# Kernel tuning notes

Measured on AMD Instinct MI355X. Metric: run time of the kernel, lower is better.

Reference implementation:

```python
import jax, jax.numpy as jnp
import numpy as np

HEADS = 16
DIM_HEAD = 64
DIM = 1024
SEQ = 2048
BATCH = 1
THR_MIN = 0.01
THR_MAX = 0.9
LN_EPS = 1e-5
NEG = -jnp.finfo(jnp.float32).max


def _ln(x, gamma):
    # torch F.layer_norm over last dim, beta fixed to zeros
    mu = jnp.mean(x, axis=-1, keepdims=True)
    var = jnp.mean(jnp.square(x - mu), axis=-1, keepdims=True)
    return (x - mu) * jax.lax.rsqrt(var + LN_EPS) * gamma


def setup_inputs() -> dict:
    key = jax.random.key(0)
    ks = jax.random.split(key, 8)
    s = 0.02  # realistic init scale for weights
    return {
        "x": jax.random.normal(ks[0], (BATCH, SEQ, DIM), jnp.float32),
        "gamma_norm": jnp.ones((DIM,), jnp.float32),
        "Wq": jax.random.normal(ks[1], (DIM, HEADS * DIM_HEAD), jnp.float32) * s,
        "Wk": jax.random.normal(ks[2], (DIM, HEADS * DIM_HEAD), jnp.float32) * s,
        "Wv": jax.random.normal(ks[3], (DIM, HEADS * DIM_HEAD), jnp.float32) * s,
        "Wout": jax.random.normal(ks[4], (HEADS * DIM_HEAD, DIM), jnp.float32) * s,
        "gamma_out": jnp.ones((DIM,), jnp.float32),
        "W_gcn0": jax.random.normal(ks[5], (DIM_HEAD, DIM_HEAD), jnp.float32) * s,
        "b_gcn0": jnp.zeros((DIM_HEAD,), jnp.float32),
        "W_gcn1": jax.random.normal(ks[6], (DIM_HEAD, DIM_HEAD), jnp.float32) * s,
        "b_gcn1": jnp.zeros((DIM_HEAD,), jnp.float32),
        "W_lin": jax.random.normal(ks[7], (DIM_HEAD, DIM_HEAD), jnp.float32) * s,
        "b_lin": jnp.zeros((DIM_HEAD,), jnp.float32),
    }


def reference(x, gamma_norm, Wq, Wk, Wv, Wout, gamma_out,
              W_gcn0, b_gcn0, W_gcn1, b_gcn1, W_lin, b_lin):
    b, n, _ = x.shape
    h, d = HEADS, DIM_HEAD
    scale = d ** -0.5

    xn = _ln(x, gamma_norm)
    # projections, split heads: b n (h d) -> b h n d
    q = (xn @ Wq).reshape(b, n, h, d).transpose(0, 2, 1, 3) * scale
    k = (xn @ Wk).reshape(b, n, h, d).transpose(0, 2, 1, 3)
    v = (xn @ Wv).reshape(b, n, h, d).transpose(0, 2, 1, 3)

    sim = jnp.einsum("bhid,bhjd->bhij", q, k)
    causal_mask = jnp.triu(jnp.ones((n, n), bool), 1)
    sim = jnp.where(causal_mask, NEG, sim)
    attn = jax.nn.softmax(sim.astype(jnp.float32), axis=-1)  # [b,h,n,n]

    out = jnp.einsum("bhij,bhjd->bhid", attn, v)

    # --- attention-derived adjacency GCN path ---
    adj = attn.reshape(b * h, n, n) + jnp.eye(n, dtype=attn.dtype)
    adj = jnp.clip(adj, 0.0, 1.0)
    adj = jnp.where(adj < THR_MIN, 0.0, adj)
    adj = jnp.where(adj > THR_MAX, 1.0, adj)

    g = v.reshape(b * h, n, d)
    deg = jnp.sum(adj, axis=-1, keepdims=True)  # [bh, n, 1]
    # GCN layer 0 (skip connection, exact GELU like nn.GELU())
    g = jax.nn.gelu(jnp.matmul(adj, g @ W_gcn0 + b_gcn0) / deg + g, approximate=False)
    # GCN layer 1
    g = jax.nn.gelu(jnp.matmul(adj, g @ W_gcn1 + b_gcn1) / deg + g, approximate=False)
    # final linear (dropout inactive in eval)
    g = g @ W_lin + b_lin

    out = out + g.reshape(b, h, n, d)

    # merge heads: b h n d -> b n (h d), output projection + LayerNorm
    out = out.transpose(0, 2, 1, 3).reshape(b, n, h * d)
    out = _ln(out @ Wout, gamma_out)
    return out
```

## Files before the change

### kernel.cpp

```cpp
#include <hip/hip_runtime.h>
#include <hip/hip_bf16.h>
#include <math.h>
#include <stdint.h>

#define DEV __device__ __forceinline__

typedef unsigned short u16;
typedef __attribute__((ext_vector_type(8))) short s16x8;
typedef __attribute__((ext_vector_type(4))) float f32x4;
typedef __attribute__((ext_vector_type(16))) float f32x16;
typedef __attribute__((ext_vector_type(4))) unsigned u32x4;

static constexpr int SEQ = 2048;
static constexpr int DIM = 1024;
static constexpr int HEADS = 16;
static constexpr int QKVLD = 3072;
static constexpr int TOT32 = 2080;

DEV u16 f2bf(float f) {
  unsigned u = __float_as_uint(f);
  u = u + 0x7FFFu + ((u >> 16) & 1u);
  return (u16)(u >> 16);
}
DEV float bf2f(u16 b) { return __uint_as_float(((unsigned)b) << 16); }
DEV float gelu_exact(float x) { return 0.5f * x * (1.0f + erff(x * 0.70710678118654752f)); }

DEV unsigned pkbf(float lo, float hi) {
  __hip_bfloat162 h = __float22bfloat162_rn(make_float2(lo, hi));
  unsigned r; __builtin_memcpy(&r, &h, 4); return r;
}

#define MFMA16(a, b, c) __builtin_amdgcn_mfma_f32_16x16x32_bf16(a, b, c, 0, 0, 0)
#define MFMA32(a, b, c) __builtin_amdgcn_mfma_f32_32x32x16_bf16(a, b, c, 0, 0, 0)

DEV s16x8 u4_to_s8(u32x4 u) { union { u32x4 a; s16x8 b; } c; c.a = u; return c.b; }

DEV float tsum16(const float* v) {
  float a0 = v[0] + v[1], a1 = v[2] + v[3], a2 = v[4] + v[5], a3 = v[6] + v[7];
  float a4 = v[8] + v[9], a5 = v[10] + v[11], a6 = v[12] + v[13], a7 = v[14] + v[15];
  float b0 = a0 + a1, b1 = a2 + a3, b2 = a4 + a5, b3 = a6 + a7;
  return (b0 + b1) + (b2 + b3);
}
DEV float tsum8(const float* v) {
  float a0 = v[0] + v[1], a1 = v[2] + v[3], a2 = v[4] + v[5], a3 = v[6] + v[7];
  return (a0 + a1) + (a2 + a3);
}

DEV void build_frags(const float* p, int hi, s16x8* fr) {
  unsigned pw[4][2];
#pragma unroll
  for (int rq = 0; rq < 4; ++rq) {
    pw[rq][0] = pkbf(p[4 * rq + 0], p[4 * rq + 1]);
    pw[rq][1] = pkbf(p[4 * rq + 2], p[4 * rq + 3]);
  }
#pragma unroll
  for (int m = 0; m < 2; ++m) {
    unsigned x0 = __shfl_xor(pw[2 * m + 1][0], 32);
    unsigned x1 = __shfl_xor(pw[2 * m + 1][1], 32);
    unsigned y0 = __shfl_xor(pw[2 * m][0], 32);
    unsigned y1 = __shfl_xor(pw[2 * m][1], 32);
    u32x4 u;
    u[0] = hi ? x0 : pw[2 * m][0];
    u[1] = hi ? x1 : pw[2 * m][1];
    u[2] = hi ? pw[2 * m + 1][0] : y0;
    u[3] = hi ? pw[2 * m + 1][1] : y1;
    fr[m] = u4_to_s8(u);
  }
}

__global__ __launch_bounds__(256) void ln_rows_f32(const float* __restrict__ in,
                                                   const float* __restrict__ gamma,
                                                   float* __restrict__ outp) {
  int row = blockIdx.x;
  const float* x = in + (size_t)row * DIM;
  float v[4];
  float s = 0.f;
#pragma unroll
  for (int e = 0; e < 4; ++e) { v[e] = x[threadIdx.x + 256 * e]; s += v[e]; }
  __shared__ float red[8];
  int lane = threadIdx.x & 63, wid = threadIdx.x >> 6;
#pragma unroll
  for (int off = 32; off; off >>= 1) s += __shfl_xor(s, off);
  if (lane == 0) red[wid] = s;
  __syncthreads();
  float mean = (red[0] + red[1] + red[2] + red[3]) * (1.0f / DIM);
  float vs = 0.f;
#pragma unroll
  for (int e = 0; e < 4; ++e) { float d = v[e] - mean; vs += d * d; }
#pragma unroll
  for (int off = 32; off; off >>= 1) vs += __shfl_xor(vs, off);
  __syncthreads();
  if (lane == 0) red[wid] = vs;
  __syncthreads();
  float var = (red[0] + red[1] + red[2] + red[3]) * (1.0f / DIM);
  float rstd = rsqrtf(var + 1e-5f);
#pragma unroll
  for (int e = 0; e < 4; ++e) {
    int c = threadIdx.x + 256 * e;
    outp[(size_t)row * DIM + c] = (v[e] - mean) * rstd * gamma[c];
  }
}

__global__ __launch_bounds__(256) void prep1(
    const float* __restrict__ x, const float* __restrict__ gamma_n, u16* __restrict__ xn,
    const float* __restrict__ Wq, const float* __restrict__ Wk, const float* __restrict__ Wv,
    const float* __restrict__ Wout, const float* __restrict__ Wg0,
    const float* __restrict__ Wg1, const float* __restrict__ Wlin,
    u16* __restrict__ WqkvT, u16* __restrict__ WoT,
    u16* __restrict__ Wg0T, u16* __restrict__ Wg1T, u16* __restrict__ WlinT) {
  int bid = blockIdx.x;
  __shared__ float tile[64][65];
  __shared__ float red[8];
  if (bid < 2048) {
    int row = bid;
    const float* xr = x + (size_t)row * DIM;
    float v[4];
    float s = 0.f;
#pragma unroll
    for (int e = 0; e < 4; ++e) { v[e] = xr[threadIdx.x + 256 * e]; s += v[e]; }
    int lane = threadIdx.x & 63, wid = threadIdx.x >> 6;
#pragma unroll
    for (int off = 32; off; off >>= 1) s += __shfl_xor(s, off);
    if (lane == 0) red[wid] = s;
    __syncthreads();
    float mean = (red[0] + red[1] + red[2] + red[3]) * (1.0f / DIM);
    float vs = 0.f;
#pragma unroll
    for (int e = 0; e < 4; ++e) { float d = v[e] - mean; vs += d * d; }
#pragma unroll
    for (int off = 32; off; off >>= 1) vs += __shfl_xor(vs, off);
    __syncthreads();
    if (lane == 0) red[wid] = vs;
    __syncthreads();
    float var = (red[0] + red[1] + red[2] + red[3]) * (1.0f / DIM);
    float rstd = rsqrtf(var + 1e-5f);
#pragma unroll
    for (int e = 0; e < 4; ++e) {
      int c = threadIdx.x + 256 * e;
      xn[(size_t)row * DIM + c] = f2bf((v[e] - mean) * rstd * gamma_n[c]);
    }
    return;
  }
  int wb = bid - 2048;
  const float* src; u16* dst; int R, C, c0, r0;
  if (wb < 1024) {
    int z = wb >> 8, rem = wb & 255;
    src = (z == 0) ? Wq : (z == 1) ? Wk : (z == 2) ? Wv : Wout;
    dst = (z == 0) ? WqkvT : (z == 1) ? WqkvT + (size_t)DIM * DIM
        : (z == 2) ? WqkvT + (size_t)2 * DIM * DIM : WoT;
    R = DIM; C = DIM; c0 = (rem & 15) * 64; r0 = (rem >> 4) * 64;
  } else {
    int k = wb - 1024;
    src = (k == 0) ? Wg0 : (k == 1) ? Wg1 : Wlin;
    dst = (k == 0) ? Wg0T : (k == 1) ? Wg1T : WlinT;
    R = 64; C = 64; c0 = 0; r0 = 0;
  }
  int tx = threadIdx.x & 63, ty = threadIdx.x >> 6;
  for (int rr = ty; rr < 64; rr += 4)
    tile[rr][tx] = src[(size_t)(r0 + rr) * C + c0 + tx];
  __syncthreads();
  for (int rr = ty; rr < 64; rr += 4)
    dst[(size_t)(c0 + rr) * R + r0 + tx] = f2bf(tile[tx][rr]);
}

__global__ __launch_bounds__(256) void prep2(
    const u16* __restrict__ QKV, u16* __restrict__ Kp, u16* __restrict__ Vp,
    const u16* __restrict__ Wg0T, const float* __restrict__ bg0, u16* __restrict__ H0p) {
  int bid = blockIdx.x;
  int tid = threadIdx.x, wid = tid >> 6, lane = tid & 63;
  __shared__ u16 t[16][72];
  __shared__ __align__(16) u16 Ws[64][72];
  __shared__ __align__(16) u16 tt[64][72];
  if (bid < 3072) {
    int bx = bid >> 4, h = bid & 15;
    int l31 = lane & 31, hi = lane >> 5;
    if (bx < 64) {
      int jb = bx, fi = wid;
      s16x8 v = *(const s16x8*)(QKV + (size_t)(jb * 32 + l31) * QKVLD + 1024 + h * 64 + fi * 16 + hi * 8);
      *(s16x8*)(Kp + ((size_t)(h * 64 + jb) * 4 + fi) * 512 + lane * 8) = v;
    } else {
      int jb16 = bx - 64;
      if (tid < 128) {
        int r = tid >> 3, c = (tid & 7) * 8;
        *(s16x8*)&t[r][c] = *(const s16x8*)(QKV + (size_t)(jb16 * 16 + r) * QKVLD + 2048 + h * 64 + c);
      }
      __syncthreads();
      if (wid < 2) {
        int dh = wid;
        s16x8 v;
#pragma unroll
        for (int e = 0; e < 8; ++e) v[e] = (short)t[hi * 8 + e][dh * 32 + l31];
        *(s16x8*)(Vp + ((size_t)(h * 128 + jb16) * 2 + dh) * 512 + lane * 8) = v;
      }
    }
    return;
  }
  int tb = bid - 3072;
  int bx = tb >> 4, h = tb & 15;
  int l15 = lane & 15, lhi = lane >> 4;
  {
    int r = tid >> 2, cc = (tid & 3) * 8;
    *(s16x8*)&Ws[r][cc] = *(const s16x8*)(Wg0T + r * 64 + cc);
    *(s16x8*)&Ws[r][cc + 32] = *(const s16x8*)(Wg0T + r * 64 + cc + 32);
  }
  __syncthreads();
  int j = bx * 64 + wid * 16 + l15;
  const u16* arow = QKV + (size_t)j * QKVLD + 2048 + h * 64;
  s16x8 a0 = *(const s16x8*)(arow + lhi * 8);
  s16x8 a1 = *(const s16x8*)(arow + 32 + lhi * 8);
  f32x4 acc[4];
#pragma unroll
  for (int c = 0; c < 4; ++c) {
    acc[c] = f32x4{0.f, 0.f, 0.f, 0.f};
    s16x8 b0 = *(const s16x8*)&Ws[c * 16 + l15][lhi * 8];
    s16x8 b1 = *(const s16x8*)&Ws[c * 16 + l15][32 + lhi * 8];
    acc[c] = MFMA16(a0, b0, acc[c]);
    acc[c] = MFMA16(a1, b1, acc[c]);
  }
  int rl = wid * 16 + lhi * 4;
#pragma unroll
  for (int c = 0; c < 4; ++c)
#pragma unroll
    for (int r = 0; r < 4; ++r)
      tt[rl + r][c * 16 + l15] = f2bf(acc[c][r] + bg0[c * 16 + l15]);
  __syncthreads();
  int l31 = lane & 31, hi = lane >> 5;
#pragma unroll
  for (int dh = 0; dh < 2; ++dh) {
    s16x8 v;
#pragma unroll
    for (int e = 0; e < 8; ++e) v[e] = (short)tt[wid * 16 + hi * 8 + e][dh * 32 + l31];
    *(s16x8*)(H0p + ((size_t)(h * 128 + bx * 4 + wid) * 2 + dh) * 512 + lane * 8) = v;
  }
}

__global__ __launch_bounds__(256) void gemm_pack(
    const u16* __restrict__ Asrc, int ld, const u16* __restrict__ Wt,
    const float* __restrict__ bias, u16* __restrict__ Hp) {
  int bx = blockIdx.x, h = blockIdx.y;
  __shared__ __align__(16) u16 Ws[64][72];
  __shared__ __align__(16) u16 tt[64][72];
  int tid = threadIdx.x, lane = tid & 63, wid = tid >> 6;
  int l15 = lane & 15, lhi = lane >> 4;
  {
    int r = tid >> 2, cc = (tid & 3) * 8;
    *(s16x8*)&Ws[r][cc] = *(const s16x8*)(Wt + r * 64 + cc);
    *(s16x8*)&Ws[r][cc + 32] = *(const s16x8*)(Wt + r * 64 + cc + 32);
  }
  __syncthreads();
  int j = bx * 64 + wid * 16 + l15;
  const u16* arow = Asrc + (size_t)j * ld + h * 64;
  s16x8 a0 = *(const s16x8*)(arow + lhi * 8);
  s16x8 a1 = *(const s16x8*)(arow + 32 + lhi * 8);
  f32x4 acc[4];
#pragma unroll
  for (int c = 0; c < 4; ++c) {
    acc[c] = f32x4{0.f, 0.f, 0.f, 0.f};
    s16x8 b0 = *(const s16x8*)&Ws[c * 16 + l15][lhi * 8];
    s16x8 b1 = *(const s16x8*)&Ws[c * 16 + l15][32 + lhi * 8];
    acc[c] = MFMA16(a0, b0, acc[c]);
    acc[c] = MFMA16(a1, b1, acc[c]);
  }
  int rl = wid * 16 + lhi * 4;
#pragma unroll
  for (int c = 0; c < 4; ++c)
#pragma unroll
    for (int r = 0; r < 4; ++r)
      tt[rl + r][c * 16 + l15] = f2bf(acc[c][r] + bias[c * 16 + l15]);
  __syncthreads();
  int l31 = lane & 31, hi = lane >> 5;
#pragma unroll
  for (int dh = 0; dh < 2; ++dh) {
    s16x8 v;
#pragma unroll
    for (int e = 0; e < 8; ++e) v[e] = (short)tt[wid * 16 + hi * 8 + e][dh * 32 + l31];
    *(s16x8*)(Hp + ((size_t)(h * 128 + bx * 4 + wid) * 2 + dh) * 512 + lane * 8) = v;
  }
}

DEV void gload_lds16(const u16* g, u16* l) {
  __builtin_amdgcn_global_load_lds(
      (const __attribute__((address_space(1))) unsigned int*)g,
      (__attribute__((address_space(3))) unsigned int*)(unsigned int)(uintptr_t)l,
      16, 0, 0);
}
template<int BM, int BN, bool OUT_F32>
__global__ __launch_bounds__(256) void gemm_t(const u16* __restrict__ A,
                                              const u16* __restrict__ Bt,
                                              void* __restrict__ Cout,
                                              int Nn, int K, int Nq, float qs) {
  constexpr int MI = BM / 32;
  constexpr int NI = BN / 32;
  __shared__ __align__(16) u16 As[BM][64];
  __shared__ __align__(16) u16 Bs[BN][64];
  int tid = threadIdx.x, lane = tid & 63, wid = tid >> 6;
  int l15 = lane & 15, lhi = lane >> 4;
  int nwg = gridDim.x * gridDim.y;
  int flat = blockIdx.y * gridDim.x + blockIdx.x;
  int q8 = nwg >> 3, r8 = nwg & 7;
  int xcd = flat & 7, idx = flat >> 3;
  int wg = (xcd < r8) ? xcd * (q8 + 1) + idx : r8 * (q8 + 1) + (xcd - r8) * q8 + idx;
  int bx = wg % gridDim.x, by = wg / gridDim.x;
  int n0 = bx * BN, m0 = by * BM;
  int wr = wid >> 1, wc = wid & 1;
  float scale = (n0 < Nq) ? qs : 1.0f;
  f32x4 acc[MI][NI];
#pragma unroll
  for (int mi = 0; mi < MI; ++mi)
#pragma unroll
    for (int ni = 0; ni < NI; ++ni) acc[mi][ni] = f32x4{0.f, 0.f, 0.f, 0.f};
  int srow = lane >> 3;
  int scol = ((lane & 7) ^ srow) * 8;
  for (int k0 = 0; k0 < K; k0 += 64) {
    __syncthreads();
#pragma unroll
    for (int i = 0; i < BM / 32; ++i) {
      int row0 = (wid * (BM / 32) + i) * 8;
      gload_lds16(A + (size_t)(m0 + row0 + srow) * K + k0 + scol, &As[row0][0]);
    }
#pragma unroll
    for (int i = 0; i < BN / 32; ++i) {
      int row0 = (wid * (BN / 32) + i) * 8;
      gload_lds16(Bt + (size_t)(n0 + row0 + srow) * K + k0 + scol, &Bs[row0][0]);
    }
    __syncthreads();
#pragma unroll
    for (int ks = 0; ks < 2; ++ks) {
      s16x8 af[MI], bf[NI];
#pragma unroll
      for (int mi = 0; mi < MI; ++mi) {
        int row = wr * (BM / 2) + mi * 16 + l15;
        int c8 = (ks * 4 + lhi) ^ (row & 7);
        af[mi] = *(const s16x8*)&As[row][c8 * 8];
      }
#pragma unroll
      for (int ni = 0; ni < NI; ++ni) {
        int row = wc * (BN / 2) + ni * 16 + l15;
        int c8 = (ks * 4 + lhi) ^ (row & 7);
        bf[ni] = *(const s16x8*)&Bs[row][c8 * 8];
      }
#pragma unroll
      for (int mi = 0; mi < MI; ++mi)
#pragma unroll
        for (int ni = 0; ni < NI; ++ni)
          acc[mi][ni] = MFMA16(af[mi], bf[ni], acc[mi][ni]);
    }
  }
  int orow0 = m0 + wr * (BM / 2), ocol0 = n0 + wc * (BN / 2);
#pragma unroll
  for (int mi = 0; mi < MI; ++mi)
#pragma unroll
    for (int ni = 0; ni < NI; ++ni)
#pragma unroll
      for (int r = 0; r < 4; ++r) {
        int row = orow0 + mi * 16 + lhi * 4 + r;
        int col = ocol0 + ni * 16 + l15;
        float vv = acc[mi][ni][r] * scale;
        if (OUT_F32) ((float*)Cout)[(size_t)row * Nn + col] = vv;
        else         ((u16*)Cout)[(size_t)row * Nn + col] = f2bf(vv);
      }
}

__global__ __launch_bounds__(256) void small_gemm_add(
    const u16* __restrict__ A, int ldo, const u16* __restrict__ Wt,
    const float* __restrict__ bias, const u16* __restrict__ addsrc,
    u16* __restrict__ outp) {
  __shared__ __align__(16) u16 Ws[64][72];
  int tid = threadIdx.x, lane = tid & 63, wid = tid >> 6;
  int l15 = lane & 15, lhi = lane >> 4;
  int m0 = blockIdx.x * 64;
  {
    int r = tid >> 2, cc = (tid & 3) * 8;
    *(s16x8*)&Ws[r][cc] = *(const s16x8*)(Wt + r * 64 + cc);
    *(s16x8*)&Ws[r][cc + 32] = *(const s16x8*)(Wt + r * 64 + cc + 32);
  }
  __syncthreads();
  int R = m0 + wid * 16 + l15;
  const u16* arow = A + (size_t)(R >> 4) * ldo + (R & 15) * 64;
  s16x8 a0 = *(const s16x8*)(arow + lhi * 8);
  s16x8 a1 = *(const s16x8*)(arow + 32 + lhi * 8);
  f32x4 acc[4];
#pragma unroll
  for (int c = 0; c < 4; ++c) {
    acc[c] = f32x4{0.f, 0.f, 0.f, 0.f};
    s16x8 b0 = *(const s16x8*)&Ws[c * 16 + l15][lhi * 8];
    s16x8 b1 = *(const s16x8*)&Ws[c * 16 + l15][32 + lhi * 8];
    acc[c] = MFMA16(a0, b0, acc[c]);
    acc[c] = MFMA16(a1, b1, acc[c]);
  }
  int orow = m0 + wid * 16 + lhi * 4;
#pragma unroll
  for (int c = 0; c < 4; ++c)
#pragma unroll
    for (int r = 0; r < 4; ++r) {
      int col = c * 16 + l15;
      size_t idx = (size_t)(orow + r) * 64 + col;
      outp[idx] = f2bf(acc[c][r] + bias[col] + bf2f(addsrc[idx]));
    }
}

static constexpr float NEGB = -3.0e38f;
DEV int crowf(int r, int hi) { return (r & 3) + 8 * (r >> 2) + 4 * hi; }

__global__ __launch_bounds__(512, 4) void attn_ss(
    const u16* __restrict__ QKV, const u16* __restrict__ Kp, const u16* __restrict__ Vp,
    float* __restrict__ lbuf, u16* __restrict__ oatt, u16* __restrict__ pfS) {
  int tid = threadIdx.x, wq = tid >> 6, lane = tid & 63;
  int l31 = lane & 31, hi = lane >> 5;
  int h = blockIdx.x & 15, sidx = blockIdx.x >> 4;
  int s = 63 - sidx;

  __shared__ float cmb[4][2][16][64];
  __shared__ float slf[8][32];
  __shared__ float sinv[32];

  int qbase = s * 32;
  int cums = (s * (s + 1)) >> 1;
  int n = s + 1;
  int c_lo = (n * wq) >> 3, c_hi = (n * (wq + 1)) >> 3;

  s16x8 qf[4];
#pragma unroll
  for (int fi = 0; fi < 4; ++fi)
    qf[fi] = *(const s16x8*)(QKV + (size_t)(qbase + l31) * QKVLD + h * 64 + fi * 16 + hi * 8);

  f32x16 pv0, pv1;
#pragma unroll
  for (int r = 0; r < 16; ++r) { pv0[r] = 0.f; pv1[r] = 0.f; }
  float lp = 0.f;
  for (int jb = c_lo; jb < c_hi; ++jb) {
    f32x16 sa;
#pragma unroll
    for (int r = 0; r < 16; ++r) sa[r] = 0.f;
#pragma unroll
    for (int fi = 0; fi < 4; ++fi) {
      s16x8 kf = *(const s16x8*)(Kp + ((size_t)(h * 64 + jb) * 4 + fi) * 512 + lane * 8);
      sa = MFMA32(kf, qf[fi], sa);
    }
    bool diag = (jb == s);
    float p[16];
#pragma unroll
    for (int r = 0; r < 16; ++r) {
      float v = sa[r];
      if (diag && (crowf(r, hi) > l31)) v = NEGB;
      p[r] = __expf(v);
    }
    lp += tsum16(p);
    s16x8 pf[2]; build_frags(p, hi, pf);
    size_t fb = ((size_t)h * TOT32 + cums + jb) * 2;
    *(s16x8*)(pfS + fb * 512 + lane * 8) = pf[0];
    *(s16x8*)(pfS + (fb + 1) * 512 + lane * 8) = pf[1];
#pragma unroll
    for (int m = 0; m < 2; ++m) {
      const u16* vb = Vp + ((size_t)(h * 128 + jb * 2 + m) * 2) * 512;
      pv0 = MFMA32(pf[m], *(const s16x8*)(vb + lane * 8), pv0);
      pv1 = MFMA32(pf[m], *(const s16x8*)(vb + 512 + lane * 8), pv1);
    }
  }
  lp += __shfl_xor(lp, 32);
  if (hi == 0) slf[wq][l31] = lp;
  __syncthreads();
  float lt = (slf[0][l31] + slf[1][l31]) + (slf[2][l31] + slf[3][l31]) +
             (slf[4][l31] + slf[5][l31]) + (slf[6][l31] + slf[7][l31]);
  if (wq == 0 && hi == 0) {
    lbuf[(size_t)h * SEQ + qbase + l31] = lt;
    sinv[l31] = 1.0f / lt;
  }
  if (wq >= 4) {
#pragma unroll
    for (int r = 0; r < 16; ++r) {
      cmb[wq - 4][0][r][lane] = pv0[r];
      cmb[wq - 4][1][r][lane] = pv1[r];
    }
  }
  __syncthreads();
  if (wq < 4) {
#pragma unroll
    for (int r = 0; r < 16; ++r) {
      pv0[r] += cmb[wq][0][r][lane];
      pv1[r] += cmb[wq][1][r][lane];
    }
  }
  __syncthreads();
  if (wq == 2 || wq == 3) {
#pragma unroll
    for (int r = 0; r < 16; ++r) {
      cmb[wq - 2][0][r][lane] = pv0[r];
      cmb[wq - 2][1][r][lane] = pv1[r];
    }
  }
  __syncthreads();
  if (wq < 2) {
#pragma unroll
    for (int r = 0; r < 16; ++r) {
      pv0[r] += cmb[wq][0][r][lane];
      pv1[r] += cmb[wq][1][r][lane];
    }
  }
  __syncthreads();
  if (wq == 1) {
#pragma unroll
    for (int r = 0; r < 16; ++r) {
      cmb[0][0][r][lane] = pv0[r];
      cmb[0][1][r][lane] = pv1[r];
    }
  }
  __syncthreads();
  if (wq == 0) {
#pragma unroll
    for (int r = 0; r < 16; ++r) {
      pv0[r] += cmb[0][0][r][lane];
      pv1[r] += cmb[0][1][r][lane];
    }
#pragma unroll
    for (int r = 0; r < 16; ++r) {
      int cr = crowf(r, hi);
      float invl = sinv[cr];
      int qr = qbase + cr;
      oatt[(size_t)qr * DIM + h * 64 + l31] = f2bf(pv0[r] * invl);
      oatt[(size_t)qr * DIM + h * 64 + 32 + l31] = f2bf(pv1[r] * invl);
    }
  }
}

__global__ __launch_bounds__(512, 4) void adjgcn1(
    const u16* __restrict__ QKV, const u16* __restrict__ H0p, u16* __restrict__ adjS,
    const float* __restrict__ lbuf, float* __restrict__ degb,
    unsigned char* __restrict__ maskb, u16* __restrict__ g1) {
  int tid = threadIdx.x, wq = tid >> 6, lane = tid & 63;
  int l31 = lane & 31, hi = lane >> 5;
  int h = blockIdx.x & 15, sidx = blockIdx.x >> 4;
  int s = 63 - sidx;

  __shared__ float cmb[4][2][16][64];
  __shared__ float sdg[8][32];
  __shared__ float sdegf[32];

  int qbase = s * 32;
  int cums = (s * (s + 1)) >> 1;
  int n = s + 1;
  int c_lo = (n * wq) >> 3, c_hi = (n * (wq + 1)) >> 3;

  float invl = 1.0f / lbuf[(size_t)h * SEQ + qbase + l31];

  f32x16 gc0, gc1;
#pragma unroll
  for (int r = 0; r < 16; ++r) { gc0[r] = 0.f; gc1[r] = 0.f; }
  float dacc = 0.f;
  for (int jb = c_lo; jb < c_hi; ++jb) {
    size_t fb = ((size_t)h * TOT32 + cums + jb) * 2;
    s16x8 f0 = *(const s16x8*)(adjS + fb * 512 + lane * 8);
    s16x8 f1 = *(const s16x8*)(adjS + (fb + 1) * 512 + lane * 8);
    bool diag = (jb == s);
    float t0[8], t1[8];
#pragma unroll
    for (int e = 0; e < 8; ++e) {
      float p0 = bf2f((u16)f0[e]) * invl;
      float p1 = bf2f((u16)f1[e]) * invl;
      t0[e] = (p0 < 0.01f) ? 0.f : ((p0 > 0.9f) ? 1.f : p0);
      t1[e] = (p1 < 0.01f) ? 0.f : ((p1 > 0.9f) ? 1.f : p1);
    }
    if (diag) {
#pragma unroll
      for (int e = 0; e < 8; ++e) {
        if (hi * 8 + e == l31) t0[e] = 1.f;
        if (16 + hi * 8 + e == l31) t1[e] = 1.f;
      }
    }
    float as0 = tsum8(t0), as1 = tsum8(t1);
    dacc += as0 + as1;
    unsigned flags = (__ballot(as0 > 0.f) ? 1u : 0u) | (__ballot(as1 > 0.f) ? 2u : 0u);
    s16x8 a0, a1;
#pragma unroll
    for (int e = 0; e < 8; ++e) { a0[e] = (short)f2bf(t0[e]); a1[e] = (short)f2bf(t1[e]); }
    if (flags & 1u) {
      *(s16x8*)(adjS + fb * 512 + lane * 8) = a0;
      const u16* hb = H0p + ((size_t)(h * 128 + jb * 2) * 2) * 512;
      gc0 = MFMA32(a0, *(const s16x8*)(hb + lane * 8), gc0);
      gc1 = MFMA32(a0, *(const s16x8*)(hb + 512 + lane * 8), gc1);
    }
    if (flags & 2u) {
      *(s16x8*)(adjS + (fb + 1) * 512 + lane * 8) = a1;
      const u16* hb = H0p + ((size_t)(h * 128 + jb * 2 + 1) * 2) * 512;
      gc0 = MFMA32(a1, *(const s16x8*)(hb + lane * 8), gc0);
      gc1 = MFMA32(a1, *(const s16x8*)(hb + 512 + lane * 8), gc1);
    }
    if (lane == 0) maskb[(size_t)h * TOT32 + cums + jb] = (unsigned char)flags;
  }
  dacc += __shfl_xor(dacc, 32);
  if (hi == 0) sdg[wq][l31] = dacc;
  if (wq >= 4) {
#pragma unroll
    for (int r = 0; r < 16; ++r) {
      cmb[wq - 4][0][r][lane] = gc0[r];
      cmb[wq - 4][1][r][lane] = gc1[r];
    }
  }
  __syncthreads();
  if (wq < 4) {
#pragma unroll
    for (int r = 0; r < 16; ++r) {
      gc0[r] += cmb[wq][0][r][lane];
      gc1[r] += cmb[wq][1][r][lane];
    }
  }
  __syncthreads();
  if (wq == 2 || wq == 3) {
#pragma unroll
    for (int r = 0; r < 16; ++r) {
      cmb[wq - 2][0][r][lane] = gc0[r];
      cmb[wq - 2][1][r][lane] = gc1[r];
    }
  }
  __syncthreads();
  if (wq < 2) {
#pragma unroll
    for (int r = 0; r < 16; ++r) {
      gc0[r] += cmb[wq][0][r][lane];
      gc1[r] += cmb[wq][1][r][lane];
    }
  }
  __syncthreads();
  if (wq == 1) {
#pragma unroll
    for (int r = 0; r < 16; ++r) {
      cmb[0][0][r][lane] = gc0[r];
      cmb[0][1][r][lane] = gc1[r];
    }
  }
  __syncthreads();
  if (wq == 0) {
    if (hi == 0) {
      float dt = 0.f;
#pragma unroll
      for (int w2 = 0; w2 < 8; ++w2) dt += sdg[w2][l31];
      sdegf[l31] = dt;
      degb[(size_t)h * SEQ + qbase + l31] = dt;
    }
  }
  __syncthreads();
  if (wq == 0) {
#pragma unroll
    for (int r = 0; r < 16; ++r) {
      gc0[r] += cmb[0][0][r][lane];
      gc1[r] += cmb[0][1][r][lane];
    }
#pragma unroll
    for (int r = 0; r < 16; ++r) {
      int cr = crowf(r, hi);
      int qr = qbase + cr;
      float dinv = 1.0f / sdegf[cr];
      float sk0 = bf2f(QKV[(size_t)qr * QKVLD + 2048 + h * 64 + l31]);
      float sk1 = bf2f(QKV[(size_t)qr * QKVLD + 2048 + h * 64 + 32 + l31]);
      g1[(size_t)qr * DIM + h * 64 + l31] = f2bf(gelu_exact(gc0[r] * dinv + sk0));
      g1[(size_t)qr * DIM + h * 64 + 32 + l31] = f2bf(gelu_exact(gc1[r] * dinv + sk1));
    }
  }
}

template<bool READ_ADJ>
__global__ __launch_bounds__(512, 4) void gcn_apply(
    const u16* __restrict__ QKV, const u16* __restrict__ Kp,
    const u16* __restrict__ Hp, const u16* __restrict__ adjS,
    const unsigned char* __restrict__ maskb,
    const float* __restrict__ lbuf, const float* __restrict__ degb,
    const u16* __restrict__ skip, int skipld, u16* __restrict__ outp) {
  int tid = threadIdx.x, wq = tid >> 6, lane = tid & 63;
  int l31 = lane & 31, hi = lane >> 5;
  int h = blockIdx.x & 15, sidx = blockIdx.x >> 4;
  int s = 63 - sidx;

  __shared__ float cmb[4][2][16][64];

  int qbase = s * 32;
  int cums = (s * (s + 1)) >> 1;
  int n = s + 1;
  int c_lo = (n * wq) >> 3, c_hi = (n * (wq + 1)) >> 3;

  f32x16 gc0, gc1;
#pragma unroll
  for (int r = 0; r < 16; ++r) { gc0[r] = 0.f; gc1[r] = 0.f; }

  if constexpr (READ_ADJ) {
    for (int jb = c_lo; jb < c_hi; ++jb) {
      unsigned flags = maskb[(size_t)h * TOT32 + cums + jb];
      if (!flags) continue;
      size_t fb = ((size_t)h * TOT32 + cums + jb) * 2;
#pragma unroll
      for (int m = 0; m < 2; ++m) if ((flags >> m) & 1u) {
        s16x8 af = *(const s16x8*)(adjS + (fb + m) * 512 + lane * 8);
        const u16* hb = Hp + ((size_t)(h * 128 + jb * 2 + m) * 2) * 512;
        gc0 = MFMA32(af, *(const s16x8*)(hb + lane * 8), gc0);
        gc1 = MFMA32(af, *(const s16x8*)(hb + 512 + lane * 8), gc1);
      }
    }
  } else {
    s16x8 qf[4];
#pragma unroll
    for (int fi = 0; fi < 4; ++fi)
      qf[fi] = *(const s16x8*)(QKV + (size_t)(qbase + l31) * QKVLD + h * 64 + fi * 16 + hi * 8);
    float invl = 1.0f / lbuf[(size_t)h * SEQ + qbase + l31];
    for (int jb = c_lo; jb < c_hi; ++jb) {
      unsigned flags = maskb[(size_t)h * TOT32 + cums + jb];
      if (!flags) continue;
      f32x16 sa;
#pragma unroll
      for (int r = 0; r < 16; ++r) sa[r] = 0.f;
#pragma unroll
      for (int fi = 0; fi < 4; ++fi) {
        s16x8 kf = *(const s16x8*)(Kp + ((size_t)(h * 64 + jb) * 4 + fi) * 512 + lane * 8);
        sa = MFMA32(kf, qf[fi], sa);
      }
      bool diag = (jb == s);
      float p[16];
#pragma unroll
      for (int r = 0; r < 16; ++r) {
        int cr = crowf(r, hi);
        float v = sa[r];
        if (diag && (cr > l31)) v = NEGB;
        float pp = __expf(v) * invl;
        p[r] = (diag && (cr == l31)) ? 1.f
               : ((pp < 0.01f) ? 0.f : ((pp > 0.9f) ? 1.f : pp));
      }
      s16x8 af[2]; build_frags(p, hi, af);
#pragma unroll
      for (int m = 0; m < 2; ++m) if ((flags >> m) & 1u) {
        const u16* hb = Hp + ((size_t)(h * 128 + jb * 2 + m) * 2) * 512;
        gc0 = MFMA32(af[m], *(const s16x8*)(hb + lane * 8), gc0);
        gc1 = MFMA32(af[m], *(const s16x8*)(hb + 512 + lane * 8), gc1);
      }
    }
  }

  if (wq >= 4) {
#pragma unroll
    for (int r = 0; r < 16; ++r) {
      cmb[wq - 4][0][r][lane] = gc0[r];
      cmb[wq - 4][1][r][lane] = gc1[r];
    }
  }
  __syncthreads();
  if (wq < 4) {
#pragma unroll
    for (int r = 0; r < 16; ++r) {
      gc0[r] += cmb[wq][0][r][lane];
      gc1[r] += cmb[wq][1][r][lane];
    }
  }
  __syncthreads();
  if (wq == 2 || wq == 3) {
#pragma unroll
    for (int r = 0; r < 16; ++r) {
      cmb[wq - 2][0][r][lane] = gc0[r];
      cmb[wq - 2][1][r][lane] = gc1[r];
    }
  }
  __syncthreads();
  if (wq < 2) {
#pragma unroll
    for (int r = 0; r < 16; ++r) {
      gc0[r] += cmb[wq][0][r][lane];
      gc1[r] += cmb[wq][1][r][lane];
    }
  }
  __syncthreads();
  if (wq == 1) {
#pragma unroll
    for (int r = 0; r < 16; ++r) {
      cmb[0][0][r][lane] = gc0[r];
      cmb[0][1][r][lane] = gc1[r];
    }
  }
  __syncthreads();
  if (wq == 0) {
#pragma unroll
    for (int r = 0; r < 16; ++r) {
      gc0[r] += cmb[0][0][r][lane];
      gc1[r] += cmb[0][1][r][lane];
    }
#pragma unroll
    for (int r = 0; r < 16; ++r) {
      int qr = qbase + crowf(r, hi);
      float dinv = 1.0f / degb[(size_t)h * SEQ + qr];
      float sk0 = bf2f(skip[(size_t)qr * skipld + h * 64 + l31]);
      float sk1 = bf2f(skip[(size_t)qr * skipld + h * 64 + 32 + l31]);
      outp[(size_t)qr * DIM + h * 64 + l31] = f2bf(gelu_exact(gc0[r] * dinv + sk0));
      outp[(size_t)qr * DIM + h * 64 + 32 + l31] = f2bf(gelu_exact(gc1[r] * dinv + sk1));
    }
  }
}

__global__ __launch_bounds__(512, 4) void attn_pv_fb(
    const u16* __restrict__ QKV, const u16* __restrict__ Kp, const u16* __restrict__ Vp,
    float* __restrict__ lbuf, float* __restrict__ degb,
    u16* __restrict__ oatt, unsigned char* __restrict__ maskb) {
  int tid = threadIdx.x, wq = tid >> 6, lane = tid & 63;
  int l31 = lane & 31, hi = lane >> 5;
  int h = blockIdx.x & 15, sidx = blockIdx.x >> 4;
  int s = 63 - sidx;

  __shared__ float cmb[4][2][16][64];
  __shared__ float slf[8][32], sdg[8][32];

  int qbase = s * 32;
  int cums = (s * (s + 1)) >> 1;
  int n = s + 1;
  int c_lo = (n * wq) >> 3, c_hi = (n * (wq + 1)) >> 3;

  s16x8 qf[4];
#pragma unroll
  for (int fi = 0; fi < 4; ++fi)
    qf[fi] = *(const s16x8*)(QKV + (size_t)(qbase + l31) * QKVLD + h * 64 + fi * 16 + hi * 8);

  float lp = 0.f;
  for (int jb = c_lo; jb < c_hi; ++jb) {
    f32x16 sa;
#pragma unroll
    for (int r = 0; r < 16; ++r) sa[r] = 0.f;
#pragma unroll
    for (int fi = 0; fi < 4; ++fi) {
      s16x8 kf = *(const s16x8*)(Kp + ((size_t)(h * 64 + jb) * 4 + fi) * 512 + lane * 8);
      sa = MFMA32(kf, qf[fi], sa);
    }
    bool diag = (jb == s);
    float ev[16];
#pragma unroll
    for (int r = 0; r < 16; ++r) {
      float v = sa[r];
      if (diag && (crowf(r, hi) > l31)) v = NEGB;
      ev[r] = __expf(v);
    }
    lp += tsum16(ev);
  }
  lp += __shfl_xor(lp, 32);
  if (hi == 0) slf[wq][l31] = lp;
  __syncthreads();
  float lt = (slf[0][l31] + slf[1][l31]) + (slf[2][l31] + slf[3][l31]) +
             (slf[4][l31] + slf[5][l31]) + (slf[6][l31] + slf[7][l31]);
  float invl = 1.0f / lt;
  if (wq == 0 && hi == 0) lbuf[(size_t)h * SEQ + qbase + l31] = lt;

  f32x16 pv0, pv1;
#pragma unroll
  for (int r = 0; r < 16; ++r) { pv0[r] = 0.f; pv1[r] = 0.f; }
  float dacc = 0.f;
  for (int jb = c_lo; jb < c_hi; ++jb) {
    f32x16 sa;
#pragma unroll
    for (int r = 0; r < 16; ++r) sa[r] = 0.f;
#pragma unroll
    for (int fi = 0; fi < 4; ++fi) {
      s16x8 kf = *(const s16x8*)(Kp + ((size_t)(h * 64 + jb) * 4 + fi) * 512 + lane * 8);
      sa = MFMA32(kf, qf[fi], sa);
    }
    bool diag = (jb == s);
    float p[16];
#pragma unroll
    for (int r = 0; r < 16; ++r) {
      float v = sa[r];
      if (diag && (crowf(r, hi) > l31)) v = NEGB;
      p[r] = __expf(v) * invl;
    }
    s16x8 pf[2]; build_frags(p, hi, pf);
#pragma unroll
    for (int m = 0; m < 2; ++m) {
      const u16* vb = Vp + ((size_t)(h * 128 + jb * 2 + m) * 2) * 512;
      pv0 = MFMA32(pf[m], *(const s16x8*)(vb + lane * 8), pv0);
      pv1 = MFMA32(pf[m], *(const s16x8*)(vb + 512 + lane * 8), pv1);
    }
#pragma unroll
    for (int r = 0; r < 16; ++r) {
      float pp = p[r];
      p[r] = (diag && (crowf(r, hi) == l31)) ? 1.f
             : ((pp < 0.01f) ? 0.f : ((pp > 0.9f) ? 1.f : pp));
    }
    float as0 = tsum8(&p[0]);
    float as1 = tsum8(&p[8]);
    dacc += as0 + as1;
    unsigned flags = (__ballot(as0 > 0.f) ? 1u : 0u) | (__ballot(as1 > 0.f) ? 2u : 0u);
    if (lane == 0) maskb[(size_t)h * TOT32 + cums + jb] = (unsigned char)flags;
  }
  dacc += __shfl_xor(dacc, 32);
  if (hi == 0) sdg[wq][l31] = dacc;
  if (wq >= 4) {
#pragma unroll
    for (int r = 0; r < 16; ++r) {
      cmb[wq - 4][0][r][lane] = pv0[r];
      cmb[wq - 4][1][r][lane] = pv1[r];
    }
  }
  __syncthreads();
  if (wq < 4) {
#pragma unroll
    for (int r = 0; r < 16; ++r) {
      pv0[r] += cmb[wq][0][r][lane];
      pv1[r] += cmb[wq][1][r][lane];
    }
  }
  __syncthreads();
  if (wq == 2 || wq == 3) {
#pragma unroll
    for (int r = 0; r < 16; ++r) {
      cmb[wq - 2][0][r][lane] = pv0[r];
      cmb[wq - 2][1][r][lane] = pv1[r];
    }
  }
  __syncthreads();
  if (wq < 2) {
#pragma unroll
    for (int r = 0; r < 16; ++r) {
      pv0[r] += cmb[wq][0][r][lane];
      pv1[r] += cmb[wq][1][r][lane];
    }
  }
  __syncthreads();
  if (wq == 1) {
#pragma unroll
    for (int r = 0; r < 16; ++r) {
      cmb[0][0][r][lane] = pv0[r];
      cmb[0][1][r][lane] = pv1[r];
    }
  }
  __syncthreads();
  if (wq == 0) {
    if (hi == 0) {
      float dt = 0.f;
#pragma unroll
      for (int w2 = 0; w2 < 8; ++w2) dt += sdg[w2][l31];
      degb[(size_t)h * SEQ + qbase + l31] = dt;
    }
#pragma unroll
    for (int r = 0; r < 16; ++r) {
      pv0[r] += cmb[0][0][r][lane];
      pv1[r] += cmb[0][1][r][lane];
    }
#pragma unroll
    for (int r = 0; r < 16; ++r) {
      int qr = qbase + crowf(r, hi);
      oatt[(size_t)qr * DIM + h * 64 + l31] = f2bf(pv0[r]);
      oatt[(size_t)qr * DIM + h * 64 + 32 + l31] = f2bf(pv1[r]);
    }
  }
}

extern "C" void kernel_launch(void* const* d_in, const int* in_sizes, int n_in,
                              void* d_out, int out_size, void* d_ws, size_t ws_size,
                              hipStream_t stream) {
  (void)in_sizes; (void)n_in; (void)out_size;
  const float* x       = (const float*)d_in[0];
  const float* gamma_n = (const float*)d_in[1];
  const float* Wq      = (const float*)d_in[2];
  const float* Wk      = (const float*)d_in[3];
  const float* Wv      = (const float*)d_in[4];
  const float* Wout    = (const float*)d_in[5];
  const float* gamma_o = (const float*)d_in[6];
  const float* Wg0     = (const float*)d_in[7];
  const float* bg0     = (const float*)d_in[8];
  const float* Wg1     = (const float*)d_in[9];
  const float* bg1     = (const float*)d_in[10];
  const float* Wlin    = (const float*)d_in[11];
  const float* blin    = (const float*)d_in[12];
  float* out = (float*)d_out;

  char* w = (char*)d_ws;
  size_t off = 0;
  auto alloc = [&](size_t bytes) -> void* {
    void* p = w + off;
    off = (off + bytes + 255) & ~(size_t)255;
    return p;
  };
  u16* xn      = (u16*)alloc((size_t)SEQ * DIM * 2);
  u16* WqkvT   = (u16*)alloc((size_t)3 * DIM * DIM * 2);
  u16* WoT     = (u16*)alloc((size_t)DIM * DIM * 2);
  u16* Wg0T    = (u16*)alloc(64 * 64 * 2);
  u16* Wg1T    = (u16*)alloc(64 * 64 * 2);
  u16* WlinT   = (u16*)alloc(64 * 64 * 2);
  u16* QKV     = (u16*)alloc((size_t)SEQ * QKVLD * 2);
  float* lbuf  = (float*)alloc((size_t)HEADS * SEQ * 4);
  float* degb  = (float*)alloc((size_t)HEADS * SEQ * 4);
  u16* oatt    = (u16*)alloc((size_t)SEQ * DIM * 2);
  u16* g1      = (u16*)alloc((size_t)SEQ * DIM * 2);
  u16* g2      = (u16*)alloc((size_t)SEQ * DIM * 2);
  u16* Kp      = (u16*)alloc((size_t)HEADS * 64 * 4 * 512 * 2);
  u16* Vp      = (u16*)alloc((size_t)HEADS * 128 * 2 * 512 * 2);
  u16* H0p     = (u16*)alloc((size_t)HEADS * 128 * 2 * 512 * 2);
  u16* H1p     = (u16*)alloc((size_t)HEADS * 128 * 2 * 512 * 2);
  u16* Om      = (u16*)alloc((size_t)SEQ * DIM * 2);
  unsigned char* maskb = (unsigned char*)alloc((size_t)HEADS * TOT32);
  float* Y     = (float*)QKV;

  size_t adj_bytes = (size_t)HEADS * TOT32 * 2 * 512 * 2;
  bool use_adj = (off + adj_bytes) <= ws_size;
  u16* adjS = use_adj ? (u16*)alloc(adj_bytes) : nullptr;

  prep1<<<2048 + 1024 + 3, 256, 0, stream>>>(x, gamma_n, xn, Wq, Wk, Wv, Wout, Wg0, Wg1, Wlin,
                                             WqkvT, WoT, Wg0T, Wg1T, WlinT);
  gemm_t<64, 128, false><<<dim3(24, 32), 256, 0, stream>>>(xn, WqkvT, QKV, QKVLD, DIM,
                                                           1024, 0.125f);
  prep2<<<3072 + 512, 256, 0, stream>>>(QKV, Kp, Vp, Wg0T, bg0, H0p);
  if (use_adj) {
    attn_ss<<<1024, 512, 0, stream>>>(QKV, Kp, Vp, lbuf, oatt, adjS);
    adjgcn1<<<1024, 512, 0, stream>>>(QKV, H0p, adjS, lbuf, degb, maskb, g1);
    gemm_pack<<<dim3(32, 16), 256, 0, stream>>>(g1, DIM, Wg1T, bg1, H1p);
    gcn_apply<true><<<1024, 512, 0, stream>>>(QKV, Kp, H1p, adjS, maskb, lbuf, degb,
                                              g1, DIM, g2);
  } else {
    attn_pv_fb<<<1024, 512, 0, stream>>>(QKV, Kp, Vp, lbuf, degb, oatt, maskb);
    gcn_apply<false><<<1024, 512, 0, stream>>>(QKV, Kp, H0p, nullptr, maskb, lbuf, degb,
                                               QKV + 2048, QKVLD, g1);
    gemm_pack<<<dim3(32, 16), 256, 0, stream>>>(g1, DIM, Wg1T, bg1, H1p);
    gcn_apply<false><<<1024, 512, 0, stream>>>(QKV, Kp, H1p, nullptr, maskb, lbuf, degb,
                                               g1, DIM, g2);
  }
  small_gemm_add<<<512, 256, 0, stream>>>(g2, DIM, WlinT, blin, oatt, Om);
  gemm_t<64, 64, true><<<dim3(16, 32), 256, 0, stream>>>(Om, WoT, Y, DIM, DIM, 0, 1.0f);
  ln_rows_f32<<<SEQ, 256, 0, stream>>>(Y, gamma_o, out);
}
```

Measured before the change: 131.7 us.

## Recompute QK^T scores in adjacency GCN kernel instead of storing unnormalized probabilities

attn_ss no longer writes the bf16 exp(scores) fragments to the adjS workspace. adjgcn1_rc instead recomputes Q·K^T with MFMA, applies exp, normalization and thresholding, and only writes the surviving adjacency fragments. This trades one full write plus read of the causal probability buffer for extra MFMA and exp work. The fallback path is also reworked so it reuses attn_ss and runs a degree-only kernel, adjdeg_fb.

```diff
diff --git a/kernel.cpp b/kernel.cpp
--- a/kernel.cpp
+++ b/kernel.cpp
@@ -404,7 +404,7 @@
 
 __global__ __launch_bounds__(512, 4) void attn_ss(
     const u16* __restrict__ QKV, const u16* __restrict__ Kp, const u16* __restrict__ Vp,
-    float* __restrict__ lbuf, u16* __restrict__ oatt, u16* __restrict__ pfS) {
+    float* __restrict__ lbuf, u16* __restrict__ oatt) {
   int tid = threadIdx.x, wq = tid >> 6, lane = tid & 63;
   int l31 = lane & 31, hi = lane >> 5;
   int h = blockIdx.x & 15, sidx = blockIdx.x >> 4;
@@ -415,7 +415,6 @@
   __shared__ float sinv[32];
 
   int qbase = s * 32;
-  int cums = (s * (s + 1)) >> 1;
   int n = s + 1;
   int c_lo = (n * wq) >> 3, c_hi = (n * (wq + 1)) >> 3;
 
@@ -447,9 +446,6 @@
     }
     lp += tsum16(p);
     s16x8 pf[2]; build_frags(p, hi, pf);
-    size_t fb = ((size_t)h * TOT32 + cums + jb) * 2;
-    *(s16x8*)(pfS + fb * 512 + lane * 8) = pf[0];
-    *(s16x8*)(pfS + (fb + 1) * 512 + lane * 8) = pf[1];
 #pragma unroll
     for (int m = 0; m < 2; ++m) {
       const u16* vb = Vp + ((size_t)(h * 128 + jb * 2 + m) * 2) * 512;
@@ -523,9 +519,9 @@
   }
 }
 
-__global__ __launch_bounds__(512, 4) void adjgcn1(
-    const u16* __restrict__ QKV, const u16* __restrict__ H0p, u16* __restrict__ adjS,
-    const float* __restrict__ lbuf, float* __restrict__ degb,
+__global__ __launch_bounds__(512, 4) void adjgcn1_rc(
+    const u16* __restrict__ QKV, const u16* __restrict__ Kp, const u16* __restrict__ H0p,
+    u16* __restrict__ adjS, const float* __restrict__ lbuf, float* __restrict__ degb,
     unsigned char* __restrict__ maskb, u16* __restrict__ g1) {
   int tid = threadIdx.x, wq = tid >> 6, lane = tid & 63;
   int l31 = lane & 31, hi = lane >> 5;
@@ -541,6 +537,10 @@
   int n = s + 1;
   int c_lo = (n * wq) >> 3, c_hi = (n * (wq + 1)) >> 3;
 
+  s16x8 qf[4];
+#pragma unroll
+  for (int fi = 0; fi < 4; ++fi)
+    qf[fi] = *(const s16x8*)(QKV + (size_t)(qbase + l31) * QKVLD + h * 64 + fi * 16 + hi * 8);
   float invl = 1.0f / lbuf[(size_t)h * SEQ + qbase + l31];
 
   f32x16 gc0, gc1;
@@ -548,42 +548,39 @@
   for (int r = 0; r < 16; ++r) { gc0[r] = 0.f; gc1[r] = 0.f; }
   float dacc = 0.f;
   for (int jb = c_lo; jb < c_hi; ++jb) {
-    size_t fb = ((size_t)h * TOT32 + cums + jb) * 2;
-    s16x8 f0 = *(const s16x8*)(adjS + fb * 512 + lane * 8);
-    s16x8 f1 = *(const s16x8*)(adjS + (fb + 1) * 512 + lane * 8);
+    f32x16 sa;
+#pragma unroll
+    for (int r = 0; r < 16; ++r) sa[r] = 0.f;
+#pragma unroll
+    for (int fi = 0; fi < 4; ++fi) {
+      s16x8 kf = *(const s16x8*)(Kp + ((size_t)(h * 64 + jb) * 4 + fi) * 512 + lane * 8);
+      sa = MFMA32(kf, qf[fi], sa);
+    }
     bool diag = (jb == s);
-    float t0[8], t1[8];
-#pragma unroll
-    for (int e = 0; e < 8; ++e) {
-      float p0 = bf2f((u16)f0[e]) * invl;
-      float p1 = bf2f((u16)f1[e]) * invl;
-      t0[e] = (p0 < 0.01f) ? 0.f : ((p0 > 0.9f) ? 1.f : p0);
-      t1[e] = (p1 < 0.01f) ? 0.f : ((p1 > 0.9f) ? 1.f : p1);
-    }
-    if (diag) {
-#pragma unroll
-      for (int e = 0; e < 8; ++e) {
-        if (hi * 8 + e == l31) t0[e] = 1.f;
-        if (16 + hi * 8 + e == l31) t1[e] = 1.f;
-      }
-    }
-    float as0 = tsum8(t0), as1 = tsum8(t1);
+    float p[16];
+#pragma unroll
+    for (int r = 0; r < 16; ++r) {
+      int cr = crowf(r, hi);
+      float v = sa[r];
+      if (diag && (cr > l31)) v = NEGB;
+      float pp = __expf(v) * invl;
+      p[r] = (diag && (cr == l31)) ? 1.f
+             : ((pp < 0.01f) ? 0.f : ((pp > 0.9f) ? 1.f : pp));
+    }
+    float as0 = tsum8(&p[0]);
+    float as1 = tsum8(&p[8]);
     dacc += as0 + as1;
     unsigned flags = (__ballot(as0 > 0.f) ? 1u : 0u) | (__ballot(as1 > 0.f) ? 2u : 0u);
-    s16x8 a0, a1;
-#pragma unroll
-    for (int e = 0; e < 8; ++e) { a0[e] = (short)f2bf(t0[e]); a1[e] = (short)f2bf(t1[e]); }
-    if (flags & 1u) {
-      *(s16x8*)(adjS + fb * 512 + lane * 8) = a0;
-      const u16* hb = H0p + ((size_t)(h * 128 + jb * 2) * 2) * 512;
-      gc0 = MFMA32(a0, *(const s16x8*)(hb + lane * 8), gc0);
-      gc1 = MFMA32(a0, *(const s16x8*)(hb + 512 + lane * 8), gc1);
-    }
-    if (flags & 2u) {
-      *(s16x8*)(adjS + (fb + 1) * 512 + lane * 8) = a1;
-      const u16* hb = H0p + ((size_t)(h * 128 + jb * 2 + 1) * 2) * 512;
-      gc0 = MFMA32(a1, *(const s16x8*)(hb + lane * 8), gc0);
-      gc1 = MFMA32(a1, *(const s16x8*)(hb + 512 + lane * 8), gc1);
+    if (flags) {
+      s16x8 af[2]; build_frags(p, hi, af);
+      size_t fb = ((size_t)h * TOT32 + cums + jb) * 2;
+#pragma unroll
+      for (int m = 0; m < 2; ++m) if ((flags >> m) & 1u) {
+        *(s16x8*)(adjS + (fb + m) * 512 + lane * 8) = af[m];
+        const u16* hb = H0p + ((size_t)(h * 128 + jb * 2 + m) * 2) * 512;
+        gc0 = MFMA32(af[m], *(const s16x8*)(hb + lane * 8), gc0);
+        gc1 = MFMA32(af[m], *(const s16x8*)(hb + 512 + lane * 8), gc1);
+      }
     }
     if (lane == 0) maskb[(size_t)h * TOT32 + cums + jb] = (unsigned char)flags;
   }
@@ -629,14 +626,12 @@
     }
   }
   __syncthreads();
-  if (wq == 0) {
-    if (hi == 0) {
-      float dt = 0.f;
-#pragma unroll
-      for (int w2 = 0; w2 < 8; ++w2) dt += sdg[w2][l31];
-      sdegf[l31] = dt;
-      degb[(size_t)h * SEQ + qbase + l31] = dt;
-    }
+  if (wq == 0 && hi == 0) {
+    float dt = 0.f;
+#pragma unroll
+    for (int w2 = 0; w2 < 8; ++w2) dt += sdg[w2][l31];
+    sdegf[l31] = dt;
+    degb[(size_t)h * SEQ + qbase + l31] = dt;
   }
   __syncthreads();
   if (wq == 0) {
@@ -790,29 +785,25 @@
   }
 }
 
-__global__ __launch_bounds__(512, 4) void attn_pv_fb(
-    const u16* __restrict__ QKV, const u16* __restrict__ Kp, const u16* __restrict__ Vp,
-    float* __restrict__ lbuf, float* __restrict__ degb,
-    u16* __restrict__ oatt, unsigned char* __restrict__ maskb) {
+__global__ __launch_bounds__(512, 4) void adjdeg_fb(
+    const u16* __restrict__ QKV, const u16* __restrict__ Kp,
+    const float* __restrict__ lbuf, float* __restrict__ degb,
+    unsigned char* __restrict__ maskb) {
   int tid = threadIdx.x, wq = tid >> 6, lane = tid & 63;
   int l31 = lane & 31, hi = lane >> 5;
   int h = blockIdx.x & 15, sidx = blockIdx.x >> 4;
   int s = 63 - sidx;
-
-  __shared__ float cmb[4][2][16][64];
-  __shared__ float slf[8][32], sdg[8][32];
-
+  __shared__ float sdg[8][32];
   int qbase = s * 32;
   int cums = (s * (s + 1)) >> 1;
   int n = s + 1;
   int c_lo = (n * wq) >> 3, c_hi = (n * (wq + 1)) >> 3;
-
   s16x8 qf[4];
 #pragma unroll
   for (int fi = 0; fi < 4; ++fi)
     qf[fi] = *(const s16x8*)(QKV + (size_t)(qbase + l31) * QKVLD + h * 64 + fi * 16 + hi * 8);
-
-  float lp = 0.f;
+  float invl = 1.0f / lbuf[(size_t)h * SEQ + qbase + l31];
+  float dacc = 0.f;
   for (int jb = c_lo; jb < c_hi; ++jb) {
     f32x16 sa;
 #pragma unroll
@@ -823,55 +814,14 @@
       sa = MFMA32(kf, qf[fi], sa);
     }
     bool diag = (jb == s);
-    float ev[16];
-#pragma unroll
-    for (int r = 0; r < 16; ++r) {
+    float p[16];
+#pragma unroll
+    for (int r = 0; r < 16; ++r) {
+      int cr = crowf(r, hi);
       float v = sa[r];
-      if (diag && (crowf(r, hi) > l31)) v = NEGB;
-      ev[r] = __expf(v);
-    }
-    lp += tsum16(ev);
-  }
-  lp += __shfl_xor(lp, 32);
-  if (hi == 0) slf[wq][l31] = lp;
-  __syncthreads();
-  float lt = (slf[0][l31] + slf[1][l31]) + (slf[2][l31] + slf[3][l31]) +
-             (slf[4][l31] + slf[5][l31]) + (slf[6][l31] + slf[7][l31]);
-  float invl = 1.0f / lt;
-  if (wq == 0 && hi == 0) lbuf[(size_t)h * SEQ + qbase + l31] = lt;
-
-  f32x16 pv0, pv1;
-#pragma unroll
-  for (int r = 0; r < 16; ++r) { pv0[r] = 0.f; pv1[r] = 0.f; }
-  float dacc = 0.f;
-  for (int jb = c_lo; jb < c_hi; ++jb) {
-    f32x16 sa;
-#pragma unroll
-    for (int r = 0; r < 16; ++r) sa[r] = 0.f;
-#pragma unroll
-    for (int fi = 0; fi < 4; ++fi) {
-      s16x8 kf = *(const s16x8*)(Kp + ((size_t)(h * 64 + jb) * 4 + fi) * 512 + lane * 8);
-      sa = MFMA32(kf, qf[fi], sa);
-    }
-    bool diag = (jb == s);
-    float p[16];
-#pragma unroll
-    for (int r = 0; r < 16; ++r) {
-      float v = sa[r];
-      if (diag && (crowf(r, hi) > l31)) v = NEGB;
-      p[r] = __expf(v) * invl;
-    }
-    s16x8 pf[2]; build_frags(p, hi, pf);
-#pragma unroll
-    for (int m = 0; m < 2; ++m) {
-      const u16* vb = Vp + ((size_t)(h * 128 + jb * 2 + m) * 2) * 512;
-      pv0 = MFMA32(pf[m], *(const s16x8*)(vb + lane * 8), pv0);
-      pv1 = MFMA32(pf[m], *(const s16x8*)(vb + 512 + lane * 8), pv1);
-    }
-#pragma unroll
-    for (int r = 0; r < 16; ++r) {
-      float pp = p[r];
-      p[r] = (diag && (crowf(r, hi) == l31)) ? 1.f
+      if (diag && (cr > l31)) v = NEGB;
+      float pp = __expf(v) * invl;
+      p[r] = (diag && (cr == l31)) ? 1.f
              : ((pp < 0.01f) ? 0.f : ((pp > 0.9f) ? 1.f : pp));
     }
     float as0 = tsum8(&p[0]);
@@ -882,64 +832,12 @@
   }
   dacc += __shfl_xor(dacc, 32);
   if (hi == 0) sdg[wq][l31] = dacc;
-  if (wq >= 4) {
-#pragma unroll
-    for (int r = 0; r < 16; ++r) {
-      cmb[wq - 4][0][r][lane] = pv0[r];
-      cmb[wq - 4][1][r][lane] = pv1[r];
-    }
-  }
-  __syncthreads();
-  if (wq < 4) {
-#pragma unroll
-    for (int r = 0; r < 16; ++r) {
-      pv0[r] += cmb[wq][0][r][lane];
-      pv1[r] += cmb[wq][1][r][lane];
-    }
-  }
-  __syncthreads();
-  if (wq == 2 || wq == 3) {
-#pragma unroll
-    for (int r = 0; r < 16; ++r) {
-      cmb[wq - 2][0][r][lane] = pv0[r];
-      cmb[wq - 2][1][r][lane] = pv1[r];
-    }
-  }
-  __syncthreads();
-  if (wq < 2) {
-#pragma unroll
-    for (int r = 0; r < 16; ++r) {
-      pv0[r] += cmb[wq][0][r][lane];
-      pv1[r] += cmb[wq][1][r][lane];
-    }
-  }
-  __syncthreads();
-  if (wq == 1) {
-#pragma unroll
-    for (int r = 0; r < 16; ++r) {
-      cmb[0][0][r][lane] = pv0[r];
-      cmb[0][1][r][lane] = pv1[r];
-    }
-  }
-  __syncthreads();
-  if (wq == 0) {
-    if (hi == 0) {
-      float dt = 0.f;
-#pragma unroll
-      for (int w2 = 0; w2 < 8; ++w2) dt += sdg[w2][l31];
-      degb[(size_t)h * SEQ + qbase + l31] = dt;
-    }
-#pragma unroll
-    for (int r = 0; r < 16; ++r) {
-      pv0[r] += cmb[0][0][r][lane];
-      pv1[r] += cmb[0][1][r][lane];
-    }
-#pragma unroll
-    for (int r = 0; r < 16; ++r) {
-      int qr = qbase + crowf(r, hi);
-      oatt[(size_t)qr * DIM + h * 64 + l31] = f2bf(pv0[r]);
-      oatt[(size_t)qr * DIM + h * 64 + 32 + l31] = f2bf(pv1[r]);
-    }
+  __syncthreads();
+  if (wq == 0 && hi == 0) {
+    float dt = 0.f;
+#pragma unroll
+    for (int w2 = 0; w2 < 8; ++w2) dt += sdg[w2][l31];
+    degb[(size_t)h * SEQ + qbase + l31] = dt;
   }
 }
 
@@ -998,14 +896,14 @@
   gemm_t<64, 128, false><<<dim3(24, 32), 256, 0, stream>>>(xn, WqkvT, QKV, QKVLD, DIM,
                                                            1024, 0.125f);
   prep2<<<3072 + 512, 256, 0, stream>>>(QKV, Kp, Vp, Wg0T, bg0, H0p);
+  attn_ss<<<1024, 512, 0, stream>>>(QKV, Kp, Vp, lbuf, oatt);
   if (use_adj) {
-    attn_ss<<<1024, 512, 0, stream>>>(QKV, Kp, Vp, lbuf, oatt, adjS);
-    adjgcn1<<<1024, 512, 0, stream>>>(QKV, H0p, adjS, lbuf, degb, maskb, g1);
+    adjgcn1_rc<<<1024, 512, 0, stream>>>(QKV, Kp, H0p, adjS, lbuf, degb, maskb, g1);
     gemm_pack<<<dim3(32, 16), 256, 0, stream>>>(g1, DIM, Wg1T, bg1, H1p);
     gcn_apply<true><<<1024, 512, 0, stream>>>(QKV, Kp, H1p, adjS, maskb, lbuf, degb,
                                               g1, DIM, g2);
   } else {
-    attn_pv_fb<<<1024, 512, 0, stream>>>(QKV, Kp, Vp, lbuf, degb, oatt, maskb);
+    adjdeg_fb<<<1024, 512, 0, stream>>>(QKV, Kp, lbuf, degb, maskb);
     gcn_apply<false><<<1024, 512, 0, stream>>>(QKV, Kp, H0p, nullptr, maskb, lbuf, degb,
                                                QKV + 2048, QKVLD, g1);
     gemm_pack<<<dim3(32, 16), 256, 0, stream>>>(g1, DIM, Wg1T, bg1, H1p);
```

Result: slower. 138.7 us (+5.3%).
